# Optimization experiments

Hardware: AMD Instinct MI355X
Metric: run time of the kernel (lower is better)

The kernel has to match this reference:

```python
import jax, jax.numpy as jnp
import numpy as np

B, C, N, D, K, M, E, G = 2, 64, 16384, 3, 128, 1, 262144, 3


def setup_inputs() -> dict:
    key = jax.random.key(0)
    ks = jax.random.split(key, 15)
    scale = 1.0 / (C * C)
    return {
        "x": jax.random.normal(ks[0], (B, C, N), jnp.float32),
        "nodes": jax.random.uniform(ks[1], (B, N, D), jnp.float32),
        "node_weights": jax.random.uniform(ks[2], (B, N, M), jnp.float32),
        "geo": jax.random.normal(ks[3], (B, G, N), jnp.float32),
        "directed_edges": jax.random.randint(ks[4], (B, E, 2), 0, N, jnp.int32),
        "edge_gradient_weights": 0.1 * jax.random.normal(ks[5], (B, E, D), jnp.float32),
        "modes": jax.random.normal(ks[6], (K, D, M), jnp.float32),
        "weights_c": scale * jax.random.uniform(ks[7], (C, C, K, M), jnp.float32),
        "weights_s": scale * jax.random.uniform(ks[8], (C, C, K, M), jnp.float32),
        "weights_0": scale * jax.random.uniform(ks[9], (C, C, 1, M), jnp.float32),
        "W": jax.random.normal(ks[10], (C, C), jnp.float32) / np.sqrt(C),
        "gw": jax.random.normal(ks[11], (C, C * D), jnp.float32) / np.sqrt(C * D),
        "geo_wx": jax.random.normal(ks[12], (C, G), jnp.float32) / np.sqrt(G),
        "wx": jax.random.normal(ks[13], (C, C), jnp.float32) / np.sqrt(C),
        "w2": jax.random.normal(ks[14], (C, C), jnp.float32) / np.sqrt(C),
    }


def reference(x, nodes, node_weights, geo, directed_edges, edge_gradient_weights,
              modes, weights_c, weights_s, weights_0, W, gw, geo_wx, wx, w2):
    # ---- Fourier bases: cos(kx), sin(kx), 1 -------------------------------
    temp = jnp.einsum('bxd,kdw->bxkw', nodes, modes)          # [B,N,K,M]
    bases_c, bases_s = jnp.cos(temp), jnp.sin(temp)
    b, n = temp.shape[0], temp.shape[1]
    bases_0 = jnp.ones((b, n, 1, temp.shape[3]), temp.dtype)
    nw = node_weights[:, :, None, :]                          # quadrature weights
    wb_c, wb_s, wb_0 = bases_c * nw, bases_s * nw, bases_0 * nw

    # ---- Spectral convolution (non-uniform Fourier neural layer) ----------
    x_c = jnp.einsum('bix,bxkw->bikw', x, wb_c)
    x_s = -jnp.einsum('bix,bxkw->bikw', x, wb_s)
    x_0 = jnp.einsum('bix,bxkw->bikw', x, wb_0)
    f_c = jnp.einsum('bikw,iokw->bokw', x_c, weights_c) - jnp.einsum('bikw,iokw->bokw', x_s, weights_s)
    f_s = jnp.einsum('bikw,iokw->bokw', x_s, weights_c) + jnp.einsum('bikw,iokw->bokw', x_c, weights_s)
    f_0 = jnp.einsum('bikw,iokw->bokw', x_0, weights_0)
    x1 = (jnp.einsum('bokw,bxkw->box', f_0, bases_0)
          + 2.0 * jnp.einsum('bokw,bxkw->box', f_c, bases_c)
          - 2.0 * jnp.einsum('bokw,bxkw->box', f_s, bases_s))

    # ---- Pointwise linear W ----------------------------------------------
    x2 = jnp.einsum('oi,bix->box', W, x)

    # ---- Least-squares gradient via edge gather + scatter-add -------------
    fT = jnp.transpose(x, (0, 2, 1))                          # [B,N,C]
    tgt, src = directed_edges[..., 0], directed_edges[..., 1]  # [B,E]
    f_src = jnp.take_along_axis(fT, src[:, :, None], axis=1)   # [B,E,C]
    f_tgt = jnp.take_along_axis(fT, tgt[:, :, None], axis=1)
    df = f_src - f_tgt
    # message[b,e,c,d] = w[b,e,d] * df[b,e,c], flattened c-major -> [B,E,C*D]
    msg = (df[..., :, None] * edge_gradient_weights[..., None, :]).reshape(b, tgt.shape[1], -1)
    gradf = jnp.zeros((b, n, msg.shape[-1]), msg.dtype).at[jnp.arange(b)[:, None], tgt].add(msg)
    x3 = jnp.einsum('og,bng->bon', gw, gradf)                  # [B,C,N]

    # ---- Geo embedding: w2 @ (softsign(geo_wx@geo) * (wx@x)) --------------
    h = jax.nn.soft_sign(jnp.einsum('og,bgx->box', geo_wx, geo)) * jnp.einsum('oi,bix->box', wx, x)
    x4 = jnp.einsum('oi,bix->box', w2, h)

    return jax.nn.gelu(x1 + x2 + x3 + x4, approximate=False)
```

## Files before the change

kernel.cpp:

```cpp
#include <hip/hip_runtime.h>
#include <hip/hip_fp16.h>
#include <math.h>

#define BB 2
#define CC 64
#define NN 16384
#define DD 3
#define KK 128
#define EE 262144
#define GG 3
#define PP 128
#define PP2 64
#define LL (NN/PP)
#define KTOT 576

typedef short bf16x8 __attribute__((ext_vector_type(8)));
typedef float f32x4  __attribute__((ext_vector_type(4)));

__device__ __forceinline__ short f2bf(float f) {
    unsigned u = __float_as_uint(f);
    u += 0x7FFF + ((u >> 16) & 1);
    return (short)(u >> 16);
}
__device__ __forceinline__ float bf2f(unsigned short u) {
    return __uint_as_float(((unsigned)u) << 16);
}

constexpr size_t OFF_XB   = 0;
constexpr size_t OFF_PC   = OFF_XB   + (size_t)BB*NN*32;
constexpr size_t OFF_PS   = OFF_PC   + (size_t)BB*PP*CC*KK;
constexpr size_t OFF_BIN4 = OFF_PC;
constexpr size_t OFF_AC   = OFF_PS   + (size_t)BB*PP*CC*KK;
constexpr size_t OFF_AS   = OFF_AC   + (size_t)BB*CC*KK;
constexpr size_t OFF_F0   = OFF_AS   + (size_t)BB*CC*KK;
constexpr size_t OFF_X0   = OFF_F0   + (size_t)BB*CC;
constexpr size_t OFF_CNT  = OFF_X0   + (size_t)BB*CC;
constexpr size_t OFF_OFFS = OFF_CNT  + (size_t)BB*NN;
constexpr size_t OFF_RANK = OFF_OFFS + (size_t)BB*NN;
constexpr size_t OFF_GRB  = OFF_RANK + (size_t)BB*EE;
constexpr size_t OFF_APAN = OFF_GRB  + (size_t)BB*NN*96;
constexpr size_t OFF_GWXT = OFF_APAN + (size_t)BB*KTOT*CC/2;

#define S_B0 (BB*PP2*4)
#define S_B1 (S_B0 + (BB*EE)/256)
#define S_B2 (S_B1 + BB*(NN/64))
#define S_B3 (S_B2 + BB*CC)
#define S_B4 (S_B3 + 48)
__global__ void __launch_bounds__(256) k1(const float* __restrict__ x,
                                          const float* __restrict__ nwt,
                                          const int* __restrict__ edges,
                                          const float* __restrict__ W,
                                          const float* __restrict__ gw,
                                          const float* __restrict__ geo_wx,
                                          const float* __restrict__ w2,
                                          const float* __restrict__ nodes,
                                          const float* __restrict__ modes,
                                          unsigned short* __restrict__ xB,
                                          float* __restrict__ x0,
                                          int* __restrict__ counts,
                                          int* __restrict__ rank,
                                          float* __restrict__ gwxT,
                                          short* __restrict__ ApanB,
                                          float* __restrict__ pc,
                                          float* __restrict__ ps) {
    int blk = blockIdx.x;
    int tid = threadIdx.x;
    __shared__ __align__(16) char smem[36864];
    if (blk < S_B0) {
        short* Axw = (short*)smem;
        short* Bc  = (short*)(smem + 17408);
        short* Bsn = (short*)(smem + 17408 + 8704);
        float* ndl = (float*)(smem + 17408 + 8704 + 8704);
        int bc = blk;
        int b = bc >> 8;
        int rem = bc & 255;
        int chunk2 = rem >> 2;
        int kt = rem & 3;
        int k0 = kt * 32;
        int lane = tid & 63;
        int w = tid >> 6;
        int col = lane & 15;
        int quad = lane >> 4;
        int wk = w & 1;
        int wi = w >> 1;

        f32x4 ac[2], as4[2];
#pragma unroll
        for (int it = 0; it < 2; it++)
#pragma unroll
            for (int r = 0; r < 4; r++) { ac[it][r] = 0.f; as4[it][r] = 0.f; }

        for (int h = 0; h < 2; h++) {
            int nbase = chunk2*256 + h*128;
            if (h) __syncthreads();
            for (int e = tid; e < 128*3; e += 256) ndl[e] = nodes[((size_t)b*NN + nbase)*3 + e];
#pragma unroll
            for (int s = 0; s < 8; s++) {
                int e = tid + s*256;
                int i = e >> 5, seg = e & 31;
                float4 xv = *(const float4*)&x[((size_t)b*CC + i)*NN + nbase + seg*4];
                float4 wv = *(const float4*)&nwt[(size_t)b*NN + nbase + seg*4];
                unsigned lo = (unsigned)(unsigned short)f2bf(xv.x*wv.x)
                            | ((unsigned)(unsigned short)f2bf(xv.y*wv.y) << 16);
                unsigned hi = (unsigned)(unsigned short)f2bf(xv.z*wv.z)
                            | ((unsigned)(unsigned short)f2bf(xv.w*wv.w) << 16);
                *(uint2*)&Axw[i*136 + seg*4] = make_uint2(lo, hi);
            }
            __syncthreads();
#pragma unroll
            for (int s = 0; s < 16; s++) {
                int e = tid + s*256;
                int n = e & 127, kl = e >> 7;
                int k = k0 + kl;
                float t = ndl[n*3+0]*modes[k*3+0] + ndl[n*3+1]*modes[k*3+1]
                        + ndl[n*3+2]*modes[k*3+2];
                Bc [kl*136 + n] = f2bf(__cosf(t));
                Bsn[kl*136 + n] = f2bf(__sinf(t));
            }
            __syncthreads();

            int rowB = (wk*16 + col)*136;
#pragma unroll
            for (int ns = 0; ns < 4; ns++) {
                int koff = ns*32 + quad*8;
                bf16x8 bcf = *(bf16x8*)&Bc [rowB + koff];
                bf16x8 bsf = *(bf16x8*)&Bsn[rowB + koff];
#pragma unroll
                for (int it = 0; it < 2; it++) {
                    int itile = wi*2 + it;
                    bf16x8 af = *(bf16x8*)&Axw[(itile*16 + col)*136 + koff];
                    ac[it]  = __builtin_amdgcn_mfma_f32_16x16x32_bf16(af, bcf, ac[it], 0, 0, 0);
                    as4[it] = __builtin_amdgcn_mfma_f32_16x16x32_bf16(af, bsf, as4[it], 0, 0, 0);
                }
            }
        }
        int base = (b*PP2 + chunk2)*CC;
        int kw = k0 + wk*16 + col;
#pragma unroll
        for (int it = 0; it < 2; it++) {
#pragma unroll
            for (int r = 0; r < 4; r++) {
                int i = (wi*2 + it)*16 + quad*4 + r;
                pc[(size_t)(base + i)*KK + kw] = ac[it][r];
                ps[(size_t)(base + i)*KK + kw] = as4[it][r];
            }
        }
    } else if (blk < S_B1) {
        int idx = (blk - S_B0)*256 + tid;
        int tgt = edges[(size_t)idx*2 + 0];
        int b = idx / EE;
        rank[idx] = atomicAdd(&counts[b*NN + tgt], 1);
    } else if (blk < S_B2) {
        float (*tile)[65] = (float (*)[65])smem;
        int tb = blk - S_B1;
        int b = tb / (NN/64);
        int n0 = (tb % (NN/64)) * 64;
        int c = tid & 63, r4 = tid >> 6;
        for (int rr = 0; rr < 16; rr++) {
            int i = r4*16 + rr;
            tile[i][c] = x[((size_t)b*CC + i)*NN + n0 + c];
        }
        __syncthreads();
        for (int rr = 0; rr < 16; rr++) {
            int nn = r4*16 + rr;
            xB[((size_t)b*NN + n0 + nn)*64 + c] = (unsigned short)f2bf(tile[c][nn]);
        }
    } else if (blk < S_B3) {
        float* red = (float*)smem;
        int bi = blk - S_B2;
        int b = bi >> 6, i = bi & 63;
        const float4* __restrict__ xr = (const float4*)&x[((size_t)b*CC + i)*NN];
        const float4* __restrict__ wr = (const float4*)&nwt[(size_t)b*NN];
        float s = 0.f;
        for (int t = tid; t < NN/4; t += 256) {
            float4 xv = xr[t];
            float4 wv = wr[t];
            s += xv.x*wv.x + xv.y*wv.y + xv.z*wv.z + xv.w*wv.w;
        }
        red[tid] = s;
        __syncthreads();
        for (int off = 128; off > 0; off >>= 1) {
            if (tid < off) red[tid] += red[tid+off];
            __syncthreads();
        }
        if (tid == 0) x0[b*CC + i] = red[0];
    } else {
        int idx = (blk - S_B3)*256 + tid;
        if (idx < CC*CC) {
            int j = idx>>6, o = idx&63;
            short wv  = f2bf(W[o*CC+j]);
            short w2v = f2bf(w2[o*CC+j]);
            ApanB[((size_t)(0*CC+o))*KTOT + 256 + j] = wv;
            ApanB[((size_t)(1*CC+o))*KTOT + 256 + j] = wv;
            ApanB[((size_t)(0*CC+o))*KTOT + 320 + j] = w2v;
            ApanB[((size_t)(1*CC+o))*KTOT + 320 + j] = w2v;
        }
        if (idx < CC*CC*DD) {
            int g = idx>>6, o = idx&63;
            short gv = f2bf(gw[o*(CC*DD)+g]);
            ApanB[((size_t)(0*CC+o))*KTOT + 384 + g] = gv;
            ApanB[((size_t)(1*CC+o))*KTOT + 384 + g] = gv;
        }
        if (idx < GG*CC) { int g = idx>>6, i = idx&63; gwxT[idx] = geo_wx[i*GG+g]; }
    }
}

__global__ void __launch_bounds__(256) k2(const float* __restrict__ pc, const float* __restrict__ ps,
                                          float* __restrict__ Ac, float* __restrict__ As,
                                          const int* __restrict__ counts,
                                          int* __restrict__ offsets) {
    int blk = blockIdx.x;
    int tid = threadIdx.x;
    if (blk < 1024) {
        int idx = blk*16 + (tid >> 4);
        int sub = tid & 15;
        if (idx >= BB*CC*KK) return;
        int b = idx / (CC*KK);
        int r = idx % (CC*KK);
        float sc = 0.f, ss = 0.f;
        for (int ch = sub; ch < PP2; ch += 16) {
            size_t o = ((size_t)(b*PP2 + ch)*CC)*KK + r;
            sc += pc[o]; ss += ps[o];
        }
        sc += __shfl_xor(sc, 1); sc += __shfl_xor(sc, 2);
        sc += __shfl_xor(sc, 4); sc += __shfl_xor(sc, 8);
        ss += __shfl_xor(ss, 1); ss += __shfl_xor(ss, 2);
        ss += __shfl_xor(ss, 4); ss += __shfl_xor(ss, 8);
        if (sub == 0) { Ac[idx] = sc; As[idx] = ss; }
    } else {
        int b = blk - 1024;
        __shared__ int part[256];
        int base = b*NN + tid*64;
        int s = 0;
        for (int j = 0; j < 64; j++) s += counts[base + j];
        part[tid] = s;
        __syncthreads();
        for (int off = 1; off < 256; off <<= 1) {
            int v = (tid >= off) ? part[tid - off] : 0;
            __syncthreads();
            part[tid] += v;
            __syncthreads();
        }
        int excl = part[tid] - s;
        for (int j = 0; j < 64; j++) {
            int c = counts[base + j];
            offsets[base + j] = excl;
            excl += c;
        }
    }
}

__global__ void __launch_bounds__(256) k3(const float* __restrict__ Ac, const float* __restrict__ As_,
                                          const float* __restrict__ wc, const float* __restrict__ wsw,
                                          const float* __restrict__ w0, const float* __restrict__ x0,
                                          const int* __restrict__ edges, const float* __restrict__ egw,
                                          const int* __restrict__ offs, const int* __restrict__ rank,
                                          float4* __restrict__ bin4,
                                          short* __restrict__ ApanB, float* __restrict__ f0) {
    int idx = blockIdx.x;
    int tid = threadIdx.x;
    if (idx >= BB*CC*2) {
        int e = (idx - BB*CC*2)*256 + tid;
        int b = e / EE;
        int tgt = edges[(size_t)e*2+0];
        int src = edges[(size_t)e*2+1];
        const float* __restrict__ ew = &egw[(size_t)e*3];
        float e0 = ew[0], e1 = ew[1], e2 = ew[2];
        int pos = offs[b*NN+tgt] + rank[e];
        bin4[(size_t)b*EE + pos] = make_float4(__int_as_float(src), e0, e1, e2);
        return;
    }
    int b = idx / (CC*2);
    int rem = idx % (CC*2);
    int o = rem >> 1, khalf = rem & 1;
    int kl = tid & 63, ig = tid >> 6;
    int k = khalf*64 + kl;
    float fc = 0.f, fs = 0.f;
    for (int ii = 0; ii < 16; ii++) {
        int i = ig*16 + ii;
        float a_c = Ac[(b*CC+i)*KK + k];
        float a_s = As_[(b*CC+i)*KK + k];
        float wcc = wc[((size_t)(i*CC+o))*KK + k];
        float wss = wsw[((size_t)(i*CC+o))*KK + k];
        fc += a_c*wcc + a_s*wss;
        fs += a_c*wss - a_s*wcc;
    }
    __shared__ float rc[256], rs[256];
    __shared__ float f0s[64];
    rc[tid] = fc; rs[tid] = fs;
    if (khalf == 0 && tid < 64) f0s[tid] = x0[b*CC + tid] * w0[tid*CC + o];
    __syncthreads();
    if (ig == 0) {
        fc = rc[kl] + rc[64+kl] + rc[128+kl] + rc[192+kl];
        fs = rs[kl] + rs[64+kl] + rs[128+kl] + rs[192+kl];
        unsigned pk = (unsigned)(unsigned short)f2bf(2.f*fc)
                    | ((unsigned)(unsigned short)f2bf(-2.f*fs) << 16);
        ((unsigned*)ApanB)[((size_t)(b*CC + o))*(KTOT/2) + k] = pk;
    }
    if (khalf == 0 && tid == 0) {
        float acc = 0.f;
        for (int i = 0; i < 64; i++) acc += f0s[i];
        f0[b*CC+o] = acc;
    }
}

__global__ void __launch_bounds__(512, 8) k_eg(const unsigned short* __restrict__ xB,
                                               const int* __restrict__ offsets,
                                               const float4* __restrict__ bin4,
                                               const float* __restrict__ nodes,
                                               const float* __restrict__ modes,
                                               const float* __restrict__ geo,
                                               const short* __restrict__ ApanB,
                                               const float* __restrict__ f0,
                                               const float* __restrict__ wx,
                                               const float* __restrict__ gwxT,
                                               float* __restrict__ out) {
    int blk = blockIdx.x;
    int b  = blk >> 9;
    int n0 = (blk & 511) * 32;
    int tid = threadIdx.x;
    int lane = tid & 63;
    int w = tid >> 6;
    int wr = w >> 1;
    int wc = w & 1;
    int col  = lane & 15;
    int quad = lane >> 4;
    int quad8 = quad * 8;
    int quad4 = quad * 4;

    __shared__ __align__(16) char smem[37776];
    short* As = (short*)smem;
    short* Bs = (short*)(smem + 9216);
    short* Ws = (short*)(smem + 13824);
    unsigned short* gradfL = (unsigned short*)(smem + 23040);
    float* ndl  = (float*)(smem + 36864);
    float* geo3 = (float*)(smem + 37248);
    int* soff   = (int*)(smem + 37632);

    if (tid < 96) ndl[tid]  = nodes[((size_t)b*NN + n0)*3 + tid];
    if (tid < 96) geo3[tid] = geo[((size_t)b*GG + (tid >> 5))*NN + n0 + (tid & 31)];
    if (tid >= 128 && tid < 161) {
        int idx = n0 + tid - 128;
        soff[tid - 128] = (idx < NN) ? offsets[b*NN + idx] : EE;
    }
    for (int e = tid; e < 4096; e += 512) {
        int i = e >> 6, j = e & 63;
        Ws[i*72 + j] = f2bf(wx[i*64 + j]);
    }
    f32x4 acc, xwa;
#pragma unroll
    for (int r = 0; r < 4; r++) { acc[r] = f0[b*CC + wr*16 + quad4 + r]; xwa[r] = 0.f; }
    __syncthreads();

    const unsigned short* __restrict__ xBb = xB + (size_t)b*NN*64 + lane;
    const float4* __restrict__ binb = bin4 + (size_t)b*EE;
    for (int q = 0; q < 4; q++) {
        int nl = w*4 + q;
        int js = soff[nl], je = soff[nl+1];
        float a0 = 0.f, a1 = 0.f, a2 = 0.f, s0 = 0.f, s1 = 0.f, s2 = 0.f;
#pragma unroll 4
        for (int j = js; j < je; j++) {
            float4 e = binb[j];
            int src = __float_as_int(e.x);
            float xs = bf2f(xBb[(size_t)src*64]);
            a0 = fmaf(xs, e.y, a0);
            a1 = fmaf(xs, e.z, a1);
            a2 = fmaf(xs, e.w, a2);
            s0 += e.y; s1 += e.z; s2 += e.w;
        }
        float xtgt = bf2f(xBb[(size_t)(n0 + nl)*64]);
        float fv0 = a0 - xtgt*s0;
        float fv1 = a1 - xtgt*s1;
        float fv2 = a2 - xtgt*s2;
        int g0 = lane*3;
        gradfL[(g0>>6)*2304 + nl*72 + (g0&63)] = (unsigned short)f2bf(fv0);
        int g1 = g0 + 1;
        gradfL[(g1>>6)*2304 + nl*72 + (g1&63)] = (unsigned short)f2bf(fv1);
        int g2 = g0 + 2;
        gradfL[(g2>>6)*2304 + nl*72 + (g2&63)] = (unsigned short)f2bf(fv2);
    }

    const short* __restrict__ Ab = ApanB + ((size_t)b*CC)*KTOT;

    for (int c = 0; c < 9; c++) {
        __syncthreads();
        {
            int o = tid >> 3, seg = tid & 7;
            *(uint4*)&As[o*72 + seg*8] =
                *(const uint4*)&Ab[(size_t)o*KTOT + c*64 + seg*8];
        }
        if (c < 4) {
#pragma unroll
            for (int s = 0; s < 2; s++) {
                int e = tid + s*512;
                int n = e >> 5, kpl = e & 31;
                int kp = c*32 + kpl;
                float t = ndl[n*3+0]*modes[kp*3+0] + ndl[n*3+1]*modes[kp*3+1]
                        + ndl[n*3+2]*modes[kp*3+2];
                unsigned pk = (unsigned)(unsigned short)f2bf(__cosf(t))
                            | ((unsigned)(unsigned short)f2bf(__sinf(t)) << 16);
                ((unsigned*)Bs)[n*36 + kpl] = pk;
            }
        } else if (c == 4) {
            if (tid < 256) {
                int n = tid >> 3, seg = tid & 7;
                *(uint4*)&Bs[n*72 + seg*8] =
                    *(const uint4*)&xB[((size_t)(b*NN + n0 + n))*64 + seg*8];
            }
        } else if (c == 5) {
            int n = wc*16 + col;
            float gv0 = geo3[n], gv1 = geo3[32+n], gv2 = geo3[64+n];
#pragma unroll
            for (int r = 0; r < 4; r++) {
                int i = wr*16 + quad4 + r;
                float t = gwxT[i]*gv0 + gwxT[64+i]*gv1 + gwxT[128+i]*gv2;
                float ssv = t / (1.f + fabsf(t));
                Bs[n*72 + i] = f2bf(ssv * xwa[r]);
            }
        }
        __syncthreads();
        const short* Bbase = (c >= 6) ? (const short*)&gradfL[(size_t)(c-6)*2304] : Bs;
        int rowA = (wr*16 + col) * 72;
        int rowB = (wc*16 + col) * 72;
#pragma unroll
        for (int ko = 0; ko < 2; ko++) {
            int koff = ko*32 + quad8;
            bf16x8 af = *(bf16x8*)&As[rowA + koff];
            bf16x8 bfv = *(bf16x8*)&Bbase[rowB + koff];
            acc = __builtin_amdgcn_mfma_f32_16x16x32_bf16(af, bfv, acc, 0, 0, 0);
            if (c == 4) {
                bf16x8 wf = *(bf16x8*)&Ws[rowA + koff];
                xwa = __builtin_amdgcn_mfma_f32_16x16x32_bf16(wf, bfv, xwa, 0, 0, 0);
            }
        }
    }
#pragma unroll
    for (int r = 0; r < 4; r++) {
        int o = wr*16 + quad4 + r;
        float v = acc[r];
        float g = 0.5f * v * (1.f + erff(v * 0.70710678118654752f));
        out[((size_t)b*CC + o)*NN + n0 + wc*16 + col] = g;
    }
}

extern "C" void kernel_launch(void* const* d_in, const int* in_sizes, int n_in,
                              void* d_out, int out_size, void* d_ws, size_t ws_size,
                              hipStream_t stream) {
    const float* x      = (const float*)d_in[0];
    const float* nodes  = (const float*)d_in[1];
    const float* nwt    = (const float*)d_in[2];
    const float* geo    = (const float*)d_in[3];
    const int*   edges  = (const int*)d_in[4];
    const float* egw    = (const float*)d_in[5];
    const float* modes  = (const float*)d_in[6];
    const float* wc     = (const float*)d_in[7];
    const float* wsw    = (const float*)d_in[8];
    const float* w0     = (const float*)d_in[9];
    const float* W      = (const float*)d_in[10];
    const float* gw     = (const float*)d_in[11];
    const float* geo_wx = (const float*)d_in[12];
    const float* wx     = (const float*)d_in[13];
    const float* w2     = (const float*)d_in[14];

    float* ws   = (float*)d_ws;
    unsigned short* xB  = (unsigned short*)(ws + OFF_XB);
    float* pc   = ws + OFF_PC;
    float* ps   = ws + OFF_PS;
    float* Ac   = ws + OFF_AC;
    float* As_  = ws + OFF_AS;
    float* f0   = ws + OFF_F0;
    float* x0   = ws + OFF_X0;
    int*  counts = (int*)(ws + OFF_CNT);
    int*  offs   = (int*)(ws + OFF_OFFS);
    int*  rank   = (int*)(ws + OFF_RANK);
    float4* bin4 = (float4*)(ws + OFF_BIN4);
    short* ApanB  = (short*)(ws + OFF_APAN);
    float* gwxT   = ws + OFF_GWXT;
    float* out  = (float*)d_out;

    hipMemsetAsync(counts, 0, (size_t)(BB*NN)*sizeof(int), stream);

    k1 <<<S_B4, 256, 0, stream>>>(x, nwt, edges, W, gw, geo_wx, w2, nodes, modes,
                                  xB, x0, counts, rank, gwxT, ApanB, pc, ps);
    k2 <<<1024 + BB, 256, 0, stream>>>(pc, ps, Ac, As_, counts, offs);
    k3 <<<BB*CC*2 + (BB*EE)/256, 256, 0, stream>>>(Ac, As_, wc, wsw, w0, x0,
                                                   edges, egw, offs, rank, bin4, ApanB, f0);
    k_eg <<<BB*(NN/32), 512, 0, stream>>>(xB, offs, bin4, nodes, modes, geo,
                                          ApanB, f0, wx, gwxT, out);
}
```

Measured before the change: 181.7 us.

## Fuse memset and three preprocessing kernels into one cooperative persistent kernel

```diff
diff --git a/kernel.cpp b/kernel.cpp
--- a/kernel.cpp
+++ b/kernel.cpp
@@ -1,6 +1,9 @@
 #include <hip/hip_runtime.h>
+#include <hip/hip_cooperative_groups.h>
 #include <hip/hip_fp16.h>
 #include <math.h>
+
+namespace cg = cooperative_groups;
 
 #define BB 2
 #define CC 64
@@ -46,261 +49,260 @@
 #define S_B2 (S_B1 + BB*(NN/64))
 #define S_B3 (S_B2 + BB*CC)
 #define S_B4 (S_B3 + 48)
-__global__ void __launch_bounds__(256) k1(const float* __restrict__ x,
-                                          const float* __restrict__ nwt,
-                                          const int* __restrict__ edges,
-                                          const float* __restrict__ W,
-                                          const float* __restrict__ gw,
-                                          const float* __restrict__ geo_wx,
-                                          const float* __restrict__ w2,
-                                          const float* __restrict__ nodes,
-                                          const float* __restrict__ modes,
-                                          unsigned short* __restrict__ xB,
-                                          float* __restrict__ x0,
-                                          int* __restrict__ counts,
-                                          int* __restrict__ rank,
-                                          float* __restrict__ gwxT,
-                                          short* __restrict__ ApanB,
-                                          float* __restrict__ pc,
-                                          float* __restrict__ ps) {
-    int blk = blockIdx.x;
+#define UB   (1024 + BB)
+#define UC   (BB*CC*2 + (BB*EE)/256)
+
+__global__ void __launch_bounds__(256)
+k123(const float* __restrict__ x, const float* __restrict__ nwt,
+     const int* __restrict__ edges, const float* __restrict__ egw,
+     const float* __restrict__ W, const float* __restrict__ gw,
+     const float* __restrict__ geo_wx, const float* __restrict__ w2,
+     const float* __restrict__ nodes, const float* __restrict__ modes,
+     const float* __restrict__ wcw, const float* __restrict__ wsw,
+     const float* __restrict__ w0,
+     unsigned short* __restrict__ xB, float* __restrict__ x0,
+     int* __restrict__ counts, int* __restrict__ rank,
+     float* __restrict__ gwxT, short* __restrict__ ApanB,
+     float* __restrict__ pc, float* __restrict__ ps,
+     float* __restrict__ Ac, float* __restrict__ As_,
+     int* __restrict__ offsets, float4* __restrict__ bin4,
+     float* __restrict__ f0) {
+    cg::grid_group gridg = cg::this_grid();
+    int NB = gridDim.x;
     int tid = threadIdx.x;
     __shared__ __align__(16) char smem[36864];
-    if (blk < S_B0) {
-        short* Axw = (short*)smem;
-        short* Bc  = (short*)(smem + 17408);
-        short* Bsn = (short*)(smem + 17408 + 8704);
-        float* ndl = (float*)(smem + 17408 + 8704 + 8704);
-        int bc = blk;
-        int b = bc >> 8;
-        int rem = bc & 255;
-        int chunk2 = rem >> 2;
-        int kt = rem & 3;
-        int k0 = kt * 32;
-        int lane = tid & 63;
-        int w = tid >> 6;
-        int col = lane & 15;
-        int quad = lane >> 4;
-        int wk = w & 1;
-        int wi = w >> 1;
-
-        f32x4 ac[2], as4[2];
-#pragma unroll
-        for (int it = 0; it < 2; it++)
-#pragma unroll
-            for (int r = 0; r < 4; r++) { ac[it][r] = 0.f; as4[it][r] = 0.f; }
-
-        for (int h = 0; h < 2; h++) {
-            int nbase = chunk2*256 + h*128;
-            if (h) __syncthreads();
-            for (int e = tid; e < 128*3; e += 256) ndl[e] = nodes[((size_t)b*NN + nbase)*3 + e];
-#pragma unroll
-            for (int s = 0; s < 8; s++) {
-                int e = tid + s*256;
-                int i = e >> 5, seg = e & 31;
-                float4 xv = *(const float4*)&x[((size_t)b*CC + i)*NN + nbase + seg*4];
-                float4 wv = *(const float4*)&nwt[(size_t)b*NN + nbase + seg*4];
-                unsigned lo = (unsigned)(unsigned short)f2bf(xv.x*wv.x)
-                            | ((unsigned)(unsigned short)f2bf(xv.y*wv.y) << 16);
-                unsigned hi = (unsigned)(unsigned short)f2bf(xv.z*wv.z)
-                            | ((unsigned)(unsigned short)f2bf(xv.w*wv.w) << 16);
-                *(uint2*)&Axw[i*136 + seg*4] = make_uint2(lo, hi);
+
+    for (int i = blockIdx.x*256 + tid; i < BB*NN; i += NB*256) counts[i] = 0;
+    gridg.sync();
+
+    for (int u = blockIdx.x; u < S_B4; u += NB) {
+        __syncthreads();
+        if (u < S_B0) {
+            short* Axw = (short*)smem;
+            short* Bc  = (short*)(smem + 17408);
+            short* Bsn = (short*)(smem + 17408 + 8704);
+            float* ndl = (float*)(smem + 17408 + 8704 + 8704);
+            int b = u >> 8;
+            int rem = u & 255;
+            int chunk2 = rem >> 2;
+            int kt = rem & 3;
+            int k0 = kt * 32;
+            int lane = tid & 63;
+            int w = tid >> 6;
+            int col = lane & 15;
+            int quad = lane >> 4;
+            int wk = w & 1;
+            int wi = w >> 1;
+
+            f32x4 ac[2], as4[2];
+#pragma unroll
+            for (int it = 0; it < 2; it++)
+#pragma unroll
+                for (int r = 0; r < 4; r++) { ac[it][r] = 0.f; as4[it][r] = 0.f; }
+
+            for (int h = 0; h < 2; h++) {
+                int nbase = chunk2*256 + h*128;
+                if (h) __syncthreads();
+                for (int e = tid; e < 128*3; e += 256) ndl[e] = nodes[((size_t)b*NN + nbase)*3 + e];
+#pragma unroll
+                for (int s = 0; s < 8; s++) {
+                    int e = tid + s*256;
+                    int i = e >> 5, seg = e & 31;
+                    float4 xv = *(const float4*)&x[((size_t)b*CC + i)*NN + nbase + seg*4];
+                    float4 wv = *(const float4*)&nwt[(size_t)b*NN + nbase + seg*4];
+                    unsigned lo = (unsigned)(unsigned short)f2bf(xv.x*wv.x)
+                                | ((unsigned)(unsigned short)f2bf(xv.y*wv.y) << 16);
+                    unsigned hi = (unsigned)(unsigned short)f2bf(xv.z*wv.z)
+                                | ((unsigned)(unsigned short)f2bf(xv.w*wv.w) << 16);
+                    *(uint2*)&Axw[i*136 + seg*4] = make_uint2(lo, hi);
+                }
+                __syncthreads();
+#pragma unroll
+                for (int s = 0; s < 16; s++) {
+                    int e = tid + s*256;
+                    int n = e & 127, kl = e >> 7;
+                    int k = k0 + kl;
+                    float t = ndl[n*3+0]*modes[k*3+0] + ndl[n*3+1]*modes[k*3+1]
+                            + ndl[n*3+2]*modes[k*3+2];
+                    Bc [kl*136 + n] = f2bf(__cosf(t));
+                    Bsn[kl*136 + n] = f2bf(__sinf(t));
+                }
+                __syncthreads();
+
+                int rowB = (wk*16 + col)*136;
+#pragma unroll
+                for (int ns = 0; ns < 4; ns++) {
+                    int koff = ns*32 + quad*8;
+                    bf16x8 bcf = *(bf16x8*)&Bc [rowB + koff];
+                    bf16x8 bsf = *(bf16x8*)&Bsn[rowB + koff];
+#pragma unroll
+                    for (int it = 0; it < 2; it++) {
+                        int itile = wi*2 + it;
+                        bf16x8 af = *(bf16x8*)&Axw[(itile*16 + col)*136 + koff];
+                        ac[it]  = __builtin_amdgcn_mfma_f32_16x16x32_bf16(af, bcf, ac[it], 0, 0, 0);
+                        as4[it] = __builtin_amdgcn_mfma_f32_16x16x32_bf16(af, bsf, as4[it], 0, 0, 0);
+                    }
+                }
+            }
+            int base = (b*PP2 + chunk2)*CC;
+            int kw = k0 + wk*16 + col;
+#pragma unroll
+            for (int it = 0; it < 2; it++) {
+#pragma unroll
+                for (int r = 0; r < 4; r++) {
+                    int i = (wi*2 + it)*16 + quad*4 + r;
+                    pc[(size_t)(base + i)*KK + kw] = ac[it][r];
+                    ps[(size_t)(base + i)*KK + kw] = as4[it][r];
+                }
+            }
+        } else if (u < S_B1) {
+            int idx = (u - S_B0)*256 + tid;
+            int tgt = edges[(size_t)idx*2 + 0];
+            int b = idx / EE;
+            rank[idx] = atomicAdd(&counts[b*NN + tgt], 1);
+        } else if (u < S_B2) {
+            float (*tile)[65] = (float (*)[65])smem;
+            int tb = u - S_B1;
+            int b = tb / (NN/64);
+            int n0 = (tb % (NN/64)) * 64;
+            int c = tid & 63, r4 = tid >> 6;
+            for (int rr = 0; rr < 16; rr++) {
+                int i = r4*16 + rr;
+                tile[i][c] = x[((size_t)b*CC + i)*NN + n0 + c];
             }
             __syncthreads();
-#pragma unroll
-            for (int s = 0; s < 16; s++) {
-                int e = tid + s*256;
-                int n = e & 127, kl = e >> 7;
-                int k = k0 + kl;
-                float t = ndl[n*3+0]*modes[k*3+0] + ndl[n*3+1]*modes[k*3+1]
-                        + ndl[n*3+2]*modes[k*3+2];
-                Bc [kl*136 + n] = f2bf(__cosf(t));
-                Bsn[kl*136 + n] = f2bf(__sinf(t));
-            }
+            for (int rr = 0; rr < 16; rr++) {
+                int nn = r4*16 + rr;
+                xB[((size_t)b*NN + n0 + nn)*64 + c] = (unsigned short)f2bf(tile[c][nn]);
+            }
+        } else if (u < S_B3) {
+            float* red = (float*)smem;
+            int bi = u - S_B2;
+            int b = bi >> 6, i = bi & 63;
+            const float4* __restrict__ xr = (const float4*)&x[((size_t)b*CC + i)*NN];
+            const float4* __restrict__ wr = (const float4*)&nwt[(size_t)b*NN];
+            float s = 0.f;
+            for (int t = tid; t < NN/4; t += 256) {
+                float4 xv = xr[t];
+                float4 wv = wr[t];
+                s += xv.x*wv.x + xv.y*wv.y + xv.z*wv.z + xv.w*wv.w;
+            }
+            red[tid] = s;
             __syncthreads();
-
-            int rowB = (wk*16 + col)*136;
-#pragma unroll
-            for (int ns = 0; ns < 4; ns++) {
-                int koff = ns*32 + quad*8;
-                bf16x8 bcf = *(bf16x8*)&Bc [rowB + koff];
-                bf16x8 bsf = *(bf16x8*)&Bsn[rowB + koff];
-#pragma unroll
-                for (int it = 0; it < 2; it++) {
-                    int itile = wi*2 + it;
-                    bf16x8 af = *(bf16x8*)&Axw[(itile*16 + col)*136 + koff];
-                    ac[it]  = __builtin_amdgcn_mfma_f32_16x16x32_bf16(af, bcf, ac[it], 0, 0, 0);
-                    as4[it] = __builtin_amdgcn_mfma_f32_16x16x32_bf16(af, bsf, as4[it], 0, 0, 0);
-                }
-            }
-        }
-        int base = (b*PP2 + chunk2)*CC;
-        int kw = k0 + wk*16 + col;
-#pragma unroll
-        for (int it = 0; it < 2; it++) {
-#pragma unroll
-            for (int r = 0; r < 4; r++) {
-                int i = (wi*2 + it)*16 + quad*4 + r;
-                pc[(size_t)(base + i)*KK + kw] = ac[it][r];
-                ps[(size_t)(base + i)*KK + kw] = as4[it][r];
-            }
-        }
-    } else if (blk < S_B1) {
-        int idx = (blk - S_B0)*256 + tid;
-        int tgt = edges[(size_t)idx*2 + 0];
-        int b = idx / EE;
-        rank[idx] = atomicAdd(&counts[b*NN + tgt], 1);
-    } else if (blk < S_B2) {
-        float (*tile)[65] = (float (*)[65])smem;
-        int tb = blk - S_B1;
-        int b = tb / (NN/64);
-        int n0 = (tb % (NN/64)) * 64;
-        int c = tid & 63, r4 = tid >> 6;
-        for (int rr = 0; rr < 16; rr++) {
-            int i = r4*16 + rr;
-            tile[i][c] = x[((size_t)b*CC + i)*NN + n0 + c];
-        }
+            for (int off = 128; off > 0; off >>= 1) {
+                if (tid < off) red[tid] += red[tid+off];
+                __syncthreads();
+            }
+            if (tid == 0) x0[b*CC + i] = red[0];
+        } else {
+            int idx = (u - S_B3)*256 + tid;
+            if (idx < CC*CC) {
+                int j = idx>>6, o = idx&63;
+                short wv  = f2bf(W[o*CC+j]);
+                short w2v = f2bf(w2[o*CC+j]);
+                ApanB[((size_t)(0*CC+o))*KTOT + 256 + j] = wv;
+                ApanB[((size_t)(1*CC+o))*KTOT + 256 + j] = wv;
+                ApanB[((size_t)(0*CC+o))*KTOT + 320 + j] = w2v;
+                ApanB[((size_t)(1*CC+o))*KTOT + 320 + j] = w2v;
+            }
+            if (idx < CC*CC*DD) {
+                int g = idx>>6, o = idx&63;
+                short gv = f2bf(gw[o*(CC*DD)+g]);
+                ApanB[((size_t)(0*CC+o))*KTOT + 384 + g] = gv;
+                ApanB[((size_t)(1*CC+o))*KTOT + 384 + g] = gv;
+            }
+            if (idx < GG*CC) { int g = idx>>6, i = idx&63; gwxT[idx] = geo_wx[i*GG+g]; }
+        }
+    }
+    gridg.sync();
+
+    for (int u = blockIdx.x; u < UB; u += NB) {
         __syncthreads();
-        for (int rr = 0; rr < 16; rr++) {
-            int nn = r4*16 + rr;
-            xB[((size_t)b*NN + n0 + nn)*64 + c] = (unsigned short)f2bf(tile[c][nn]);
-        }
-    } else if (blk < S_B3) {
-        float* red = (float*)smem;
-        int bi = blk - S_B2;
-        int b = bi >> 6, i = bi & 63;
-        const float4* __restrict__ xr = (const float4*)&x[((size_t)b*CC + i)*NN];
-        const float4* __restrict__ wr = (const float4*)&nwt[(size_t)b*NN];
-        float s = 0.f;
-        for (int t = tid; t < NN/4; t += 256) {
-            float4 xv = xr[t];
-            float4 wv = wr[t];
-            s += xv.x*wv.x + xv.y*wv.y + xv.z*wv.z + xv.w*wv.w;
-        }
-        red[tid] = s;
+        if (u < 1024) {
+            int idx = u*16 + (tid >> 4);
+            int sub = tid & 15;
+            int b = idx / (CC*KK);
+            int r = idx % (CC*KK);
+            float sc = 0.f, ss = 0.f;
+            for (int ch = sub; ch < PP2; ch += 16) {
+                size_t o = ((size_t)(b*PP2 + ch)*CC)*KK + r;
+                sc += pc[o]; ss += ps[o];
+            }
+            sc += __shfl_xor(sc, 1); sc += __shfl_xor(sc, 2);
+            sc += __shfl_xor(sc, 4); sc += __shfl_xor(sc, 8);
+            ss += __shfl_xor(ss, 1); ss += __shfl_xor(ss, 2);
+            ss += __shfl_xor(ss, 4); ss += __shfl_xor(ss, 8);
+            if (sub == 0) { Ac[idx] = sc; As_[idx] = ss; }
+        } else {
+            int b = u - 1024;
+            int* part = (int*)smem;
+            int base = b*NN + tid*64;
+            int s = 0;
+            for (int j = 0; j < 64; j++) s += counts[base + j];
+            part[tid] = s;
+            __syncthreads();
+            for (int off = 1; off < 256; off <<= 1) {
+                int v = (tid >= off) ? part[tid - off] : 0;
+                __syncthreads();
+                part[tid] += v;
+                __syncthreads();
+            }
+            int excl = part[tid] - s;
+            for (int j = 0; j < 64; j++) {
+                int c = counts[base + j];
+                offsets[base + j] = excl;
+                excl += c;
+            }
+        }
+    }
+    gridg.sync();
+
+    for (int u = blockIdx.x; u < UC; u += NB) {
         __syncthreads();
-        for (int off = 128; off > 0; off >>= 1) {
-            if (tid < off) red[tid] += red[tid+off];
+        if (u >= BB*CC*2) {
+            int e = (u - BB*CC*2)*256 + tid;
+            int b = e / EE;
+            int tgt = edges[(size_t)e*2+0];
+            int src = edges[(size_t)e*2+1];
+            const float* __restrict__ ew = &egw[(size_t)e*3];
+            float e0 = ew[0], e1 = ew[1], e2 = ew[2];
+            int pos = offsets[b*NN+tgt] + rank[e];
+            bin4[(size_t)b*EE + pos] = make_float4(__int_as_float(src), e0, e1, e2);
+        } else {
+            int b = u / (CC*2);
+            int rem = u % (CC*2);
+            int o = rem >> 1, khalf = rem & 1;
+            int kl = tid & 63, ig = tid >> 6;
+            int k = khalf*64 + kl;
+            float fc = 0.f, fs = 0.f;
+            for (int ii = 0; ii < 16; ii++) {
+                int i = ig*16 + ii;
+                float a_c = Ac[(b*CC+i)*KK + k];
+                float a_s = As_[(b*CC+i)*KK + k];
+                float wcc = wcw[((size_t)(i*CC+o))*KK + k];
+                float wss = wsw[((size_t)(i*CC+o))*KK + k];
+                fc += a_c*wcc + a_s*wss;
+                fs += a_c*wss - a_s*wcc;
+            }
+            float* rc  = (float*)smem;
+            float* rs  = (float*)(smem + 1024);
+            float* f0s = (float*)(smem + 2048);
+            rc[tid] = fc; rs[tid] = fs;
+            if (khalf == 0 && tid < 64) f0s[tid] = x0[b*CC + tid] * w0[tid*CC + o];
             __syncthreads();
-        }
-        if (tid == 0) x0[b*CC + i] = red[0];
-    } else {
-        int idx = (blk - S_B3)*256 + tid;
-        if (idx < CC*CC) {
-            int j = idx>>6, o = idx&63;
-            short wv  = f2bf(W[o*CC+j]);
-            short w2v = f2bf(w2[o*CC+j]);
-            ApanB[((size_t)(0*CC+o))*KTOT + 256 + j] = wv;
-            ApanB[((size_t)(1*CC+o))*KTOT + 256 + j] = wv;
-            ApanB[((size_t)(0*CC+o))*KTOT + 320 + j] = w2v;
-            ApanB[((size_t)(1*CC+o))*KTOT + 320 + j] = w2v;
-        }
-        if (idx < CC*CC*DD) {
-            int g = idx>>6, o = idx&63;
-            short gv = f2bf(gw[o*(CC*DD)+g]);
-            ApanB[((size_t)(0*CC+o))*KTOT + 384 + g] = gv;
-            ApanB[((size_t)(1*CC+o))*KTOT + 384 + g] = gv;
-        }
-        if (idx < GG*CC) { int g = idx>>6, i = idx&63; gwxT[idx] = geo_wx[i*GG+g]; }
-    }
-}
-
-__global__ void __launch_bounds__(256) k2(const float* __restrict__ pc, const float* __restrict__ ps,
-                                          float* __restrict__ Ac, float* __restrict__ As,
-                                          const int* __restrict__ counts,
-                                          int* __restrict__ offsets) {
-    int blk = blockIdx.x;
-    int tid = threadIdx.x;
-    if (blk < 1024) {
-        int idx = blk*16 + (tid >> 4);
-        int sub = tid & 15;
-        if (idx >= BB*CC*KK) return;
-        int b = idx / (CC*KK);
-        int r = idx % (CC*KK);
-        float sc = 0.f, ss = 0.f;
-        for (int ch = sub; ch < PP2; ch += 16) {
-            size_t o = ((size_t)(b*PP2 + ch)*CC)*KK + r;
-            sc += pc[o]; ss += ps[o];
-        }
-        sc += __shfl_xor(sc, 1); sc += __shfl_xor(sc, 2);
-        sc += __shfl_xor(sc, 4); sc += __shfl_xor(sc, 8);
-        ss += __shfl_xor(ss, 1); ss += __shfl_xor(ss, 2);
-        ss += __shfl_xor(ss, 4); ss += __shfl_xor(ss, 8);
-        if (sub == 0) { Ac[idx] = sc; As[idx] = ss; }
-    } else {
-        int b = blk - 1024;
-        __shared__ int part[256];
-        int base = b*NN + tid*64;
-        int s = 0;
-        for (int j = 0; j < 64; j++) s += counts[base + j];
-        part[tid] = s;
-        __syncthreads();
-        for (int off = 1; off < 256; off <<= 1) {
-            int v = (tid >= off) ? part[tid - off] : 0;
-            __syncthreads();
-            part[tid] += v;
-            __syncthreads();
-        }
-        int excl = part[tid] - s;
-        for (int j = 0; j < 64; j++) {
-            int c = counts[base + j];
-            offsets[base + j] = excl;
-            excl += c;
-        }
-    }
-}
-
-__global__ void __launch_bounds__(256) k3(const float* __restrict__ Ac, const float* __restrict__ As_,
-                                          const float* __restrict__ wc, const float* __restrict__ wsw,
-                                          const float* __restrict__ w0, const float* __restrict__ x0,
-                                          const int* __restrict__ edges, const float* __restrict__ egw,
-                                          const int* __restrict__ offs, const int* __restrict__ rank,
-                                          float4* __restrict__ bin4,
-                                          short* __restrict__ ApanB, float* __restrict__ f0) {
-    int idx = blockIdx.x;
-    int tid = threadIdx.x;
-    if (idx >= BB*CC*2) {
-        int e = (idx - BB*CC*2)*256 + tid;
-        int b = e / EE;
-        int tgt = edges[(size_t)e*2+0];
-        int src = edges[(size_t)e*2+1];
-        const float* __restrict__ ew = &egw[(size_t)e*3];
-        float e0 = ew[0], e1 = ew[1], e2 = ew[2];
-        int pos = offs[b*NN+tgt] + rank[e];
-        bin4[(size_t)b*EE + pos] = make_float4(__int_as_float(src), e0, e1, e2);
-        return;
-    }
-    int b = idx / (CC*2);
-    int rem = idx % (CC*2);
-    int o = rem >> 1, khalf = rem & 1;
-    int kl = tid & 63, ig = tid >> 6;
-    int k = khalf*64 + kl;
-    float fc = 0.f, fs = 0.f;
-    for (int ii = 0; ii < 16; ii++) {
-        int i = ig*16 + ii;
-        float a_c = Ac[(b*CC+i)*KK + k];
-        float a_s = As_[(b*CC+i)*KK + k];
-        float wcc = wc[((size_t)(i*CC+o))*KK + k];
-        float wss = wsw[((size_t)(i*CC+o))*KK + k];
-        fc += a_c*wcc + a_s*wss;
-        fs += a_c*wss - a_s*wcc;
-    }
-    __shared__ float rc[256], rs[256];
-    __shared__ float f0s[64];
-    rc[tid] = fc; rs[tid] = fs;
-    if (khalf == 0 && tid < 64) f0s[tid] = x0[b*CC + tid] * w0[tid*CC + o];
-    __syncthreads();
-    if (ig == 0) {
-        fc = rc[kl] + rc[64+kl] + rc[128+kl] + rc[192+kl];
-        fs = rs[kl] + rs[64+kl] + rs[128+kl] + rs[192+kl];
-        unsigned pk = (unsigned)(unsigned short)f2bf(2.f*fc)
-                    | ((unsigned)(unsigned short)f2bf(-2.f*fs) << 16);
-        ((unsigned*)ApanB)[((size_t)(b*CC + o))*(KTOT/2) + k] = pk;
-    }
-    if (khalf == 0 && tid == 0) {
-        float acc = 0.f;
-        for (int i = 0; i < 64; i++) acc += f0s[i];
-        f0[b*CC+o] = acc;
+            if (ig == 0) {
+                fc = rc[kl] + rc[64+kl] + rc[128+kl] + rc[192+kl];
+                fs = rs[kl] + rs[64+kl] + rs[128+kl] + rs[192+kl];
+                unsigned pk = (unsigned)(unsigned short)f2bf(2.f*fc)
+                            | ((unsigned)(unsigned short)f2bf(-2.f*fs) << 16);
+                ((unsigned*)ApanB)[((size_t)(b*CC + o))*(KTOT/2) + k] = pk;
+            }
+            if (khalf == 0 && tid == 0) {
+                float acc = 0.f;
+                for (int i = 0; i < 64; i++) acc += f0s[i];
+                f0[b*CC+o] = acc;
+            }
+        }
     }
 }
 
@@ -453,7 +455,7 @@
     const int*   edges  = (const int*)d_in[4];
     const float* egw    = (const float*)d_in[5];
     const float* modes  = (const float*)d_in[6];
-    const float* wc     = (const float*)d_in[7];
+    const float* wcw    = (const float*)d_in[7];
     const float* wsw    = (const float*)d_in[8];
     const float* w0     = (const float*)d_in[9];
     const float* W      = (const float*)d_in[10];
@@ -478,13 +480,26 @@
     float* gwxT   = ws + OFF_GWXT;
     float* out  = (float*)d_out;
 
-    hipMemsetAsync(counts, 0, (size_t)(BB*NN)*sizeof(int), stream);
-
-    k1 <<<S_B4, 256, 0, stream>>>(x, nwt, edges, W, gw, geo_wx, w2, nodes, modes,
-                                  xB, x0, counts, rank, gwxT, ApanB, pc, ps);
-    k2 <<<1024 + BB, 256, 0, stream>>>(pc, ps, Ac, As_, counts, offs);
-    k3 <<<BB*CC*2 + (BB*EE)/256, 256, 0, stream>>>(Ac, As_, wc, wsw, w0, x0,
-                                                   edges, egw, offs, rank, bin4, ApanB, f0);
+    static int s_nb = 0;
+    if (s_nb == 0) {
+        int bpc = 0;
+        hipError_t err = hipOccupancyMaxActiveBlocksPerMultiprocessor(
+            &bpc, (const void*)k123, 256, 0);
+        if (err != hipSuccess || bpc < 1) bpc = 1;
+        s_nb = bpc * 256;
+        if (s_nb < 1) s_nb = 1;
+    }
+
+    void* args[] = {
+        (void*)&x, (void*)&nwt, (void*)&edges, (void*)&egw,
+        (void*)&W, (void*)&gw, (void*)&geo_wx, (void*)&w2,
+        (void*)&nodes, (void*)&modes, (void*)&wcw, (void*)&wsw, (void*)&w0,
+        (void*)&xB, (void*)&x0, (void*)&counts, (void*)&rank,
+        (void*)&gwxT, (void*)&ApanB, (void*)&pc, (void*)&ps,
+        (void*)&Ac, (void*)&As_, (void*)&offs, (void*)&bin4, (void*)&f0
+    };
+    hipLaunchCooperativeKernel((const void*)k123, dim3(s_nb), dim3(256),
+                               args, 0, stream);
     k_eg <<<BB*(NN/32), 512, 0, stream>>>(xB, offs, bin4, nodes, modes, geo,
                                           ApanB, f0, wx, gwxT, out);
 }
```

Result: slower. 299.6 us (+64.9%).
